# Performance work log

Hardware: AMD Instinct MI355X
Metric: run time of the kernel (lower is better)

Reference implementation:

```python
import jax, jax.numpy as jnp
import numpy as np


def setup_inputs() -> dict:
    key = jax.random.key(0)
    k1, k2 = jax.random.split(key)
    B, N, D = 32, 1024, 384
    x = jax.random.normal(k1, (B, N, D), dtype=jnp.float32)
    durations = jax.random.randint(k2, (B, N), 0, 8, dtype=jnp.int32)
    return {"x": x, "durations": durations, "max_len": 4096}


def reference(x, durations, max_len):
    # x: (B, N, D) encoder output; durations: (B, N) frames per phoneme.
    # Fused length-regulation: for each output frame t, source phoneme index is
    # the smallest n with cumsum(durations)[n] > t (searchsorted right on cumsum).
    B, N, D = x.shape
    cum = jnp.cumsum(durations, axis=1)              # (B, N)
    total = cum[:, -1]                               # (B,) total frames per row
    t = jnp.arange(max_len, dtype=cum.dtype)         # (T,)
    # (B, T) source index per output frame
    idx = jax.vmap(lambda c: jnp.searchsorted(c, t, side="right"))(cum)
    mel_mask = t[None, :] >= total[:, None]          # (B, T) True where padding
    idx_c = jnp.minimum(idx, N - 1)                  # clamp out-of-range (padded frames)
    out = jnp.take_along_axis(x, idx_c[:, :, None], axis=1)   # (B, T, D)
    out = jnp.where(mel_mask[:, :, None], jnp.zeros((), x.dtype), out)
    return out, mel_mask
```

## Files before the change

### kernel.cpp

```cpp
#include <hip/hip_runtime.h>

#define BB 32
#define NN 1024
#define DD 384
#define ML 4096
#define D4 (DD / 4)
#define RPB 8
#define GT2 256
#define NBLK2 (BB * ML / RPB)

__global__ __launch_bounds__(NN) void lr_scan_scatter_kernel(
    const int* __restrict__ dur, int* __restrict__ idxb,
    float* __restrict__ mask) {
    __shared__ int s[NN];
    __shared__ int idx_lds[ML];
    const int b = blockIdx.x;
    const int i = threadIdx.x;

    s[i] = dur[b * NN + i];
    #pragma unroll
    for (int k = 0; k < ML / NN; ++k) idx_lds[i + k * NN] = -1;
    __syncthreads();

    #pragma unroll
    for (int off = 1; off < NN; off <<= 1) {
        int v = (i >= off) ? s[i - off] : 0;
        __syncthreads();
        s[i] += v;
        __syncthreads();
    }

    const int end_raw = s[i];
    const int start   = (i == 0) ? 0 : s[i - 1];
    const int end     = (end_raw < ML) ? end_raw : ML;
    for (int t = start; t < end; ++t) idx_lds[t] = i;
    __syncthreads();

    #pragma unroll
    for (int k = 0; k < ML / NN; ++k) {
        const int t = i + k * NN;
        const int v = idx_lds[t];
        idxb[b * ML + t] = v;
        mask[b * ML + t] = (v < 0) ? 1.0f : 0.0f;
    }
}

__global__ __launch_bounds__(GT2) void lr_copy_kernel(
    const float4* __restrict__ x, const int* __restrict__ idxb,
    float4* __restrict__ out) {
    const int g = ((blockIdx.x & 7) * (NBLK2 / 8)) + (blockIdx.x >> 3);
    const int row0 = g * RPB;
    const int tid = threadIdx.x;

    #pragma unroll
    for (int k = 0; k < 3; ++k) {
        const int pos = tid + k * GT2;
        const int r   = pos / D4;
        const int d4  = pos - r * D4;
        const int row = row0 + r;
        const int idx = idxb[row];
        float4 v = {0.0f, 0.0f, 0.0f, 0.0f};
        if (idx >= 0) {
            const int b = row >> 12;
            v = x[((b << 10) + idx) * D4 + d4];
        }
        out[(size_t)row * D4 + d4] = v;
    }
}

extern "C" void kernel_launch(void* const* d_in, const int* in_sizes, int n_in,
                              void* d_out, int out_size, void* d_ws, size_t ws_size,
                              hipStream_t stream) {
    const float* x = (const float*)d_in[0];
    const int* dur = (const int*)d_in[1];

    int* idxb   = (int*)d_ws;
    float* out  = (float*)d_out;
    float* mask = out + (size_t)BB * ML * DD;

    lr_scan_scatter_kernel<<<BB, NN, 0, stream>>>(dur, idxb, mask);
    lr_copy_kernel<<<NBLK2, GT2, 0, stream>>>(
        (const float4*)x, idxb, (float4*)out);
}
```

Measured before the change: 244.4 us.

## Fuse scan and gather into one kernel with per-block searchsorted

Replaces the two-kernel pipeline (one block per batch scanning durations and scattering indices, then a gather kernel) with a single kernel. Each block redoes the cumsum of its batch row with wave shuffles, binary-searches the source index for its 32 output frames, writes the mask, and copies the rows using nontemporal stores. This removes the second launch, the workspace index round-trip and the serial scan bottleneck. In exchange every block rescans 1024 durations, which is redundant work and adds syncs.

Measured after the change: 249.4 us. +2.1%, slower.

```diff
diff --git a/kernel.cpp b/kernel.cpp
--- a/kernel.cpp
+++ b/kernel.cpp
@@ -5,66 +5,78 @@
 #define DD 384
 #define ML 4096
 #define D4 (DD / 4)
-#define RPB 8
-#define GT2 256
-#define NBLK2 (BB * ML / RPB)
+#define RPB 32
+#define GT 256
+#define F4PT (RPB * D4 / GT)
+#define NBLK (BB * ML / RPB)
+#define NW (GT / 64)
 
-__global__ __launch_bounds__(NN) void lr_scan_scatter_kernel(
-    const int* __restrict__ dur, int* __restrict__ idxb,
-    float* __restrict__ mask) {
-    __shared__ int s[NN];
-    __shared__ int idx_lds[ML];
-    const int b = blockIdx.x;
-    const int i = threadIdx.x;
+typedef float f32x4 __attribute__((ext_vector_type(4)));
 
-    s[i] = dur[b * NN + i];
+__global__ __launch_bounds__(GT) void lr_fused_kernel(
+    const float4* __restrict__ x, const int4* __restrict__ dur4,
+    float4* __restrict__ out, float* __restrict__ mask) {
+    __shared__ __align__(16) int cum[NN];
+    __shared__ int wsum[NW];
+    __shared__ int idxs[RPB];
+
+    const int g    = ((blockIdx.x & 7) * (NBLK / 8)) + (blockIdx.x >> 3);
+    const int row0 = g * RPB;
+    const int b    = row0 >> 12;
+    const int t0   = row0 & (ML - 1);
+    const int tid  = threadIdx.x;
+    const int lane = tid & 63;
+    const int wid  = tid >> 6;
+
+    int4 d = dur4[b * (NN / 4) + tid];
+    int s = d.x + d.y + d.z + d.w;
     #pragma unroll
-    for (int k = 0; k < ML / NN; ++k) idx_lds[i + k * NN] = -1;
+    for (int off = 1; off < 64; off <<= 1) {
+        int n = __shfl_up(s, off);
+        if (lane >= off) s += n;
+    }
+    if (lane == 63) wsum[wid] = s;
+    __syncthreads();
+    int woff = 0;
+    #pragma unroll
+    for (int w = 0; w < NW - 1; ++w)
+        if (w < wid) woff += wsum[w];
+    int4 c;
+    c.w = woff + s;
+    c.z = c.w - d.w;
+    c.y = c.z - d.z;
+    c.x = c.y - d.y;
+    reinterpret_cast<int4*>(cum)[tid] = c;
+    __syncthreads();
+
+    const int total = cum[NN - 1];
+    if (tid < RPB) {
+        const int t = t0 + tid;
+        int idx = -1;
+        if (t < total) {
+            int pos = 0;
+            #pragma unroll
+            for (int step = 512; step > 0; step >>= 1) {
+                const int np = pos + step;
+                if (np <= NN && cum[np - 1] <= t) pos = np;
+            }
+            idx = (pos < NN) ? pos : NN - 1;
+        }
+        idxs[tid] = idx;
+        mask[b * ML + t] = (idx < 0) ? 1.0f : 0.0f;
+    }
     __syncthreads();
 
     #pragma unroll
-    for (int off = 1; off < NN; off <<= 1) {
-        int v = (i >= off) ? s[i - off] : 0;
-        __syncthreads();
-        s[i] += v;
-        __syncthreads();
-    }
-
-    const int end_raw = s[i];
-    const int start   = (i == 0) ? 0 : s[i - 1];
-    const int end     = (end_raw < ML) ? end_raw : ML;
-    for (int t = start; t < end; ++t) idx_lds[t] = i;
-    __syncthreads();
-
-    #pragma unroll
-    for (int k = 0; k < ML / NN; ++k) {
-        const int t = i + k * NN;
-        const int v = idx_lds[t];
-        idxb[b * ML + t] = v;
-        mask[b * ML + t] = (v < 0) ? 1.0f : 0.0f;
-    }
-}
-
-__global__ __launch_bounds__(GT2) void lr_copy_kernel(
-    const float4* __restrict__ x, const int* __restrict__ idxb,
-    float4* __restrict__ out) {
-    const int g = ((blockIdx.x & 7) * (NBLK2 / 8)) + (blockIdx.x >> 3);
-    const int row0 = g * RPB;
-    const int tid = threadIdx.x;
-
-    #pragma unroll
-    for (int k = 0; k < 3; ++k) {
-        const int pos = tid + k * GT2;
+    for (int k = 0; k < F4PT; ++k) {
+        const int pos = tid + k * GT;
         const int r   = pos / D4;
         const int d4  = pos - r * D4;
-        const int row = row0 + r;
-        const int idx = idxb[row];
+        const int idx = idxs[r];
         float4 v = {0.0f, 0.0f, 0.0f, 0.0f};
-        if (idx >= 0) {
-            const int b = row >> 12;
-            v = x[((b << 10) + idx) * D4 + d4];
-        }
-        out[(size_t)row * D4 + d4] = v;
+        if (idx >= 0) v = x[((size_t)b * NN + idx) * D4 + d4];
+        f32x4* dst = reinterpret_cast<f32x4*>(&out[(size_t)(row0 + r) * D4 + d4]);
+        __builtin_nontemporal_store(*reinterpret_cast<const f32x4*>(&v), dst);
     }
 }
 
@@ -74,11 +86,9 @@
     const float* x = (const float*)d_in[0];
     const int* dur = (const int*)d_in[1];
 
-    int* idxb   = (int*)d_ws;
     float* out  = (float*)d_out;
     float* mask = out + (size_t)BB * ML * DD;
 
-    lr_scan_scatter_kernel<<<BB, NN, 0, stream>>>(dur, idxb, mask);
-    lr_copy_kernel<<<NBLK2, GT2, 0, stream>>>(
-        (const float4*)x, idxb, (float4*)out);
+    lr_fused_kernel<<<NBLK, GT, 0, stream>>>(
+        (const float4*)x, (const int4*)dur, (float4*)out, mask);
 }
```

## Use wave-shuffle scan with int4 loads and flatten gather-copy to one float4 per thread

Applied to the files above, without the earlier changes.

The scan kernel now runs with 256 threads, each handling four durations loaded as an int4. It uses a wavefront shuffle scan plus a small cross-wave sum instead of a 1024-thread LDS Hillis-Steele scan with many barriers, and it writes idx and mask with vectorized stores. The copy kernel becomes a flat one-float4-per-thread gather with more blocks, in place of 8 rows per block with 3 iterations. The scan change cuts barrier and LDS traffic. The flat copy raises the block count and the scheduling overhead in exchange for simpler indexing.

New measurement: 251.3 us. 2.8% more time.

```diff
diff --git a/kernel.cpp b/kernel.cpp
--- a/kernel.cpp
+++ b/kernel.cpp
@@ -5,67 +5,82 @@
 #define DD 384
 #define ML 4096
 #define D4 (DD / 4)
-#define RPB 8
-#define GT2 256
-#define NBLK2 (BB * ML / RPB)
+#define TOTF4 (BB * ML * D4)
+#define CT 256
+#define NBLK (TOTF4 / CT)
 
-__global__ __launch_bounds__(NN) void lr_scan_scatter_kernel(
-    const int* __restrict__ dur, int* __restrict__ idxb,
+__global__ __launch_bounds__(CT) void lr_scan_kernel(
+    const int4* __restrict__ dur4, int* __restrict__ idxb,
     float* __restrict__ mask) {
-    __shared__ int s[NN];
-    __shared__ int idx_lds[ML];
-    const int b = blockIdx.x;
-    const int i = threadIdx.x;
+    __shared__ __align__(16) int idx_lds[ML];
+    __shared__ int wsum[CT / 64];
+    const int b    = blockIdx.x;
+    const int tid  = threadIdx.x;
+    const int lane = tid & 63;
+    const int wid  = tid >> 6;
 
-    s[i] = dur[b * NN + i];
+    int4 d = dur4[b * (NN / 4) + tid];
+    int4* lds4 = reinterpret_cast<int4*>(idx_lds);
     #pragma unroll
-    for (int k = 0; k < ML / NN; ++k) idx_lds[i + k * NN] = -1;
+    for (int k = 0; k < ML / 4 / CT; ++k)
+        lds4[tid + k * CT] = make_int4(-1, -1, -1, -1);
+
+    int s = d.x + d.y + d.z + d.w;
+    #pragma unroll
+    for (int off = 1; off < 64; off <<= 1) {
+        int n = __shfl_up(s, off);
+        if (lane >= off) s += n;
+    }
+    if (lane == 63) wsum[wid] = s;
+    __syncthreads();
+    int woff = 0;
+    #pragma unroll
+    for (int w = 0; w < CT / 64 - 1; ++w)
+        if (w < wid) woff += wsum[w];
+
+    int c3 = woff + s;
+    int c2 = c3 - d.w;
+    int c1 = c2 - d.z;
+    int c0 = c1 - d.y;
+    int p  = c0 - d.x;
+
+    const int i0 = tid * 4;
+    int lo, hi;
+    lo = p;  hi = (c0 < ML) ? c0 : ML; for (int t = lo; t < hi; ++t) idx_lds[t] = i0;
+    lo = c0; hi = (c1 < ML) ? c1 : ML; for (int t = lo; t < hi; ++t) idx_lds[t] = i0 + 1;
+    lo = c1; hi = (c2 < ML) ? c2 : ML; for (int t = lo; t < hi; ++t) idx_lds[t] = i0 + 2;
+    lo = c2; hi = (c3 < ML) ? c3 : ML; for (int t = lo; t < hi; ++t) idx_lds[t] = i0 + 3;
     __syncthreads();
 
+    int4* idxb4 = reinterpret_cast<int4*>(idxb + b * ML);
+    float4* mask4 = reinterpret_cast<float4*>(mask + b * ML);
     #pragma unroll
-    for (int off = 1; off < NN; off <<= 1) {
-        int v = (i >= off) ? s[i - off] : 0;
-        __syncthreads();
-        s[i] += v;
-        __syncthreads();
-    }
-
-    const int end_raw = s[i];
-    const int start   = (i == 0) ? 0 : s[i - 1];
-    const int end     = (end_raw < ML) ? end_raw : ML;
-    for (int t = start; t < end; ++t) idx_lds[t] = i;
-    __syncthreads();
-
-    #pragma unroll
-    for (int k = 0; k < ML / NN; ++k) {
-        const int t = i + k * NN;
-        const int v = idx_lds[t];
-        idxb[b * ML + t] = v;
-        mask[b * ML + t] = (v < 0) ? 1.0f : 0.0f;
+    for (int k = 0; k < ML / 4 / CT; ++k) {
+        const int4 v = lds4[tid + k * CT];
+        idxb4[tid + k * CT] = v;
+        float4 m;
+        m.x = (v.x < 0) ? 1.0f : 0.0f;
+        m.y = (v.y < 0) ? 1.0f : 0.0f;
+        m.z = (v.z < 0) ? 1.0f : 0.0f;
+        m.w = (v.w < 0) ? 1.0f : 0.0f;
+        mask4[tid + k * CT] = m;
     }
 }
 
-__global__ __launch_bounds__(GT2) void lr_copy_kernel(
+__global__ __launch_bounds__(CT) void lr_flat_copy_kernel(
     const float4* __restrict__ x, const int* __restrict__ idxb,
     float4* __restrict__ out) {
-    const int g = ((blockIdx.x & 7) * (NBLK2 / 8)) + (blockIdx.x >> 3);
-    const int row0 = g * RPB;
-    const int tid = threadIdx.x;
-
-    #pragma unroll
-    for (int k = 0; k < 3; ++k) {
-        const int pos = tid + k * GT2;
-        const int r   = pos / D4;
-        const int d4  = pos - r * D4;
-        const int row = row0 + r;
-        const int idx = idxb[row];
-        float4 v = {0.0f, 0.0f, 0.0f, 0.0f};
-        if (idx >= 0) {
-            const int b = row >> 12;
-            v = x[((b << 10) + idx) * D4 + d4];
-        }
-        out[(size_t)row * D4 + d4] = v;
+    const int g   = ((blockIdx.x & 7) * (NBLK / 8)) + (blockIdx.x >> 3);
+    const int gid = g * CT + threadIdx.x;
+    const int row = gid / D4;
+    const int d4  = gid - row * D4;
+    const int idx = idxb[row];
+    float4 v = {0.0f, 0.0f, 0.0f, 0.0f};
+    if (idx >= 0) {
+        const int b = row >> 12;
+        v = x[((b << 10) + idx) * D4 + d4];
     }
+    out[gid] = v;
 }
 
 extern "C" void kernel_launch(void* const* d_in, const int* in_sizes, int n_in,
@@ -78,7 +93,7 @@
     float* out  = (float*)d_out;
     float* mask = out + (size_t)BB * ML * DD;
 
-    lr_scan_scatter_kernel<<<BB, NN, 0, stream>>>(dur, idxb, mask);
-    lr_copy_kernel<<<NBLK2, GT2, 0, stream>>>(
+    lr_scan_kernel<<<BB, CT, 0, stream>>>((const int4*)dur, idxb, mask);
+    lr_flat_copy_kernel<<<NBLK, CT, 0, stream>>>(
         (const float4*)x, idxb, (float4*)out);
 }
```
